# Performance work log

Hardware: AMD Instinct MI355X
Metric: run time of the kernel (lower is better)

Reference implementation:

```python
import jax, jax.numpy as jnp
import numpy as np

N_QUBITS = 12
N_LAYERS = 2
IN_DIM = 16
BATCH = 4096
EPS = 1e-6
C64 = jnp.complex64


def _rz(t):
    return jnp.diag(jnp.stack([jnp.exp(-0.5j * t), jnp.exp(0.5j * t)]).astype(C64))


def _ry(t):
    c = jnp.cos(0.5 * t); s = jnp.sin(0.5 * t)
    return jnp.stack([jnp.stack([c, -s]), jnp.stack([s, c])]).astype(C64)


def _su2(p):
    # SU2: RZ(p0) then RY(p1) then RZ(p2)  ->  U = RZ(p2) @ RY(p1) @ RZ(p0)
    return _rz(p[2]) @ _ry(p[1]) @ _rz(p[0])


def _ising_xx(t):
    c = jnp.cos(0.5 * t).astype(C64); is_ = (-1j * jnp.sin(0.5 * t)).astype(C64)
    M = jnp.zeros((4, 4), C64)
    M = M.at[(0, 1, 2, 3), (0, 1, 2, 3)].set(c)
    M = M.at[(0, 1, 2, 3), (3, 2, 1, 0)].set(is_)
    return M


def _ising_yy(t):
    c = jnp.cos(0.5 * t).astype(C64); is_ = (-1j * jnp.sin(0.5 * t)).astype(C64)
    M = jnp.zeros((4, 4), C64)
    M = M.at[(0, 1, 2, 3), (0, 1, 2, 3)].set(c)
    M = M.at[(1, 2), (2, 1)].set(is_)
    M = M.at[(0, 3), (3, 0)].set(-is_)
    return M


def _ising_zz(t):
    sign = jnp.array([1.0, -1.0, -1.0, 1.0])
    return jnp.diag(jnp.exp(-0.5j * t * sign).astype(C64))


def _apply_1q(state, U, w):
    # state: [B] + [2]*n ; U: [2,2] (shared) or [B,2,2] (per-sample)
    st = jnp.moveaxis(state, w + 1, -1)
    if U.ndim == 2:
        st = jnp.einsum('...i,ji->...j', st, U)
    else:
        st = jnp.einsum('b...i,bji->b...j', st, U)
    return jnp.moveaxis(st, -1, w + 1)


def _apply_2q(state, U, w0, w1):
    st = jnp.moveaxis(state, (w0 + 1, w1 + 1), (-2, -1))
    shp = st.shape
    st = st.reshape(shp[:-2] + (4,))
    st = jnp.einsum('...i,ji->...j', st, U)
    return jnp.moveaxis(st.reshape(shp), (-2, -1), (w0 + 1, w1 + 1))


def _apply_zz_batched(state, theta, w0, w1):
    # IsingZZ is diagonal: multiply by per-sample phases, no matmul needed
    st = jnp.moveaxis(state, (w0 + 1, w1 + 1), (-2, -1))
    sign = jnp.array([[1.0, -1.0], [-1.0, 1.0]])
    ph = jnp.exp(-0.5j * theta[:, None, None] * sign).astype(C64)
    ph = ph.reshape((ph.shape[0],) + (1,) * (st.ndim - 3) + (2, 2))
    return jnp.moveaxis(st * ph, (-2, -1), (w0 + 1, w1 + 1))


def _forward(x, W, b, params):
    n = N_QUBITS
    B = x.shape[0]
    qfeat = x @ W.T + b  # NQE linear front-end -> [B, n_qubits] angles
    state = jnp.zeros((B, 2 ** n), C64).at[:, 0].set(1.0).reshape((B,) + (2,) * n)
    # --- data embedding (n_layers repetitions of RY + nearest-neighbor IsingZZ) ---
    c = jnp.cos(0.5 * qfeat); s = jnp.sin(0.5 * qfeat)
    for _ in range(N_LAYERS):
        for q in range(n):
            U = jnp.stack([jnp.stack([c[:, q], -s[:, q]], -1),
                           jnp.stack([s[:, q], c[:, q]], -1)], -2).astype(C64)  # [B,2,2]
            state = _apply_1q(state, U, q)
        for q in range(n - 1):
            state = _apply_zz_batched(state, qfeat[:, q] * qfeat[:, q + 1], q, q + 1)
    # --- SU4 brickwork ansatz (shared params across batch) ---
    g1 = n // 2; g2 = (n - 1) // 2
    layout = [(2 * i, 2 * i + 1) for i in range(g1)] + [(2 * i + 1, 2 * i + 2) for i in range(g2)]
    p = 0
    for a, bq in layout:
        pp = params[p:p + 15]; p += 15
        state = _apply_1q(state, _su2(pp[0:3]), a)
        state = _apply_1q(state, _su2(pp[3:6]), bq)
        state = _apply_2q(state, _ising_xx(pp[6]), a, bq)   # cartan_sign='ising'
        state = _apply_2q(state, _ising_yy(pp[7]), a, bq)
        state = _apply_2q(state, _ising_zz(pp[8]), a, bq)
        state = _apply_1q(state, _su2(pp[9:12]), a)
        state = _apply_1q(state, _su2(pp[12:15]), bq)
    state = _apply_1q(state, _su2(params[p:p + 3]), 0)
    # <Z_0> = P(q0=0) - P(q0=1)
    probs = jnp.sum(jnp.abs(state.reshape(B, 2, -1)) ** 2, axis=-1)
    y = (probs[:, 0] - probs[:, 1] + 1.0) * 0.5
    return jnp.clip(y, EPS, 1.0 - EPS)


def setup_inputs():
    key = jax.random.key(0)
    k1, k2, k3 = jax.random.split(key, 3)
    x = jax.random.normal(k1, (BATCH, IN_DIM), jnp.float32)
    W = jax.random.normal(k2, (N_QUBITS, IN_DIM), jnp.float32) * 0.3
    b = jnp.zeros((N_QUBITS,), jnp.float32)
    n_params = 15 * (N_QUBITS // 2 + (N_QUBITS - 1) // 2) + 3  # = 168
    params = jax.random.normal(k3, (n_params,), jnp.float32) * 0.1
    return {"x": x, "W": W, "b": b, "params": params}


def reference(x, W, b, params):
    return _forward(x, W, b, params)
```

## Files before the change

kernel.cpp:

```cpp
#include <hip/hip_runtime.h>
#include <math.h>

#define TPB 256

__device__ __forceinline__ float2 cmul(float2 a, float2 b) {
    return make_float2(a.x*b.x - a.y*b.y, a.x*b.y + a.y*b.x);
}
__device__ __forceinline__ float2 cadd(float2 a, float2 b) {
    return make_float2(a.x + b.x, a.y + b.y);
}
__device__ __forceinline__ float2 cfma2(float2 a, float2 b, float2 c) {
    c.x = fmaf(a.x, b.x, fmaf(-a.y, b.y, c.x));
    c.y = fmaf(a.x, b.y, fmaf( a.y, b.x, c.y));
    return c;
}

__device__ __forceinline__ void build_su2(const float* __restrict__ p, float2 U[2][2]) {
    float sb, cb;
    sincosf(0.5f * p[1], &sb, &cb);
    float ap = 0.5f * (p[0] + p[2]);
    float am = 0.5f * (p[0] - p[2]);
    float sap, cap, sam, cam;
    sincosf(ap, &sap, &cap);
    sincosf(am, &sam, &cam);
    U[0][0] = make_float2( cb * cap, -cb * sap);
    U[0][1] = make_float2(-sb * cam, -sb * sam);
    U[1][0] = make_float2( sb * cam, -sb * sam);
    U[1][1] = make_float2( cb * cap,  cb * sap);
}

__global__ __launch_bounds__(TPB) void qcnn_fused(
    const float* __restrict__ x,
    const float* __restrict__ W,
    const float* __restrict__ bias,
    const float* __restrict__ params,
    float* __restrict__ out,
    int n)
{
    __shared__ float2 sE[16];
    __shared__ float  sM[4];

    const int t   = threadIdx.x;
    const int tid = blockIdx.x * TPB + t;
    const int row = (tid < n) ? tid : (n - 1);

    const float* xr = x + row * 16;
    const float4 xv0 = *(const float4*)(xr + 0);
    const float4 xv1 = *(const float4*)(xr + 4);
    const float4 xv2 = *(const float4*)(xr + 8);
    const float4 xv3 = *(const float4*)(xr + 12);
    float qf[4];
    #pragma unroll
    for (int q = 0; q < 4; ++q) {
        const float* wr = W + q * 16;
        float acc = bias[q];
        acc = fmaf(xv0.x, wr[0],  acc); acc = fmaf(xv0.y, wr[1],  acc);
        acc = fmaf(xv0.z, wr[2],  acc); acc = fmaf(xv0.w, wr[3],  acc);
        acc = fmaf(xv1.x, wr[4],  acc); acc = fmaf(xv1.y, wr[5],  acc);
        acc = fmaf(xv1.z, wr[6],  acc); acc = fmaf(xv1.w, wr[7],  acc);
        acc = fmaf(xv2.x, wr[8],  acc); acc = fmaf(xv2.y, wr[9],  acc);
        acc = fmaf(xv2.z, wr[10], acc); acc = fmaf(xv2.w, wr[11], acc);
        acc = fmaf(xv3.x, wr[12], acc); acc = fmaf(xv3.y, wr[13], acc);
        acc = fmaf(xv3.z, wr[14], acc); acc = fmaf(xv3.w, wr[15], acc);
        qf[q] = acc;
    }
    float c[4], s[4];
    #pragma unroll
    for (int q = 0; q < 4; ++q) sincosf(0.5f * qf[q], &s[q], &c[q]);
    float zs01, zc01, zs12, zc12, zs23, zc23;
    sincosf(0.5f * qf[0] * qf[1], &zs01, &zc01);
    sincosf(0.5f * qf[1] * qf[2], &zs12, &zc12);
    sincosf(0.5f * qf[2] * qf[3], &zs23, &zc23);
    const float2 f01e = make_float2(zc01, -zs01), f01d = make_float2(zc01, zs01);
    const float2 f12e = make_float2(zc12, -zs12), f12d = make_float2(zc12, zs12);
    const float2 f23e = make_float2(zc23, -zs23), f23d = make_float2(zc23, zs23);

    if (t < 16) {
        const float* pp = params;
        float2 A1[2][2], B1[2][2], A2[2][2], B2[2][2];
        build_su2(pp + 0,  A1);
        build_su2(pp + 3,  B1);
        build_su2(pp + 9,  A2);
        build_su2(pp + 12, B2);
        const float thx = pp[6], thy = pp[7], thz = pp[8];
        float Sa, Ca, Sb, Cb, sz, cz;
        sincosf(0.5f * (thx - thy), &Sa, &Ca);
        sincosf(0.5f * (thx + thy), &Sb, &Cb);
        sincosf(0.5f * thz, &sz, &cz);
        const float2 pz  = make_float2(cz, -sz);
        const float2 pzc = make_float2(cz,  sz);
        const float2 K00 = make_float2(Ca * pz.x,  Ca * pz.y);
        const float2 K03 = cmul(make_float2(0.f, -Sa), pz);
        const float2 K11 = make_float2(Cb * pzc.x, Cb * pzc.y);
        const float2 K12 = cmul(make_float2(0.f, -Sb), pzc);

        const int r = t >> 2, cc = t & 3;
        float2 T0c[4];
        #pragma unroll
        for (int j = 0; j < 4; ++j)
            T0c[j] = cmul(A1[j >> 1][cc >> 1], B1[j & 1][cc & 1]);
        float2 M1c[4];
        M1c[0] = cadd(cmul(K00, T0c[0]), cmul(K03, T0c[3]));
        M1c[1] = cadd(cmul(K11, T0c[1]), cmul(K12, T0c[2]));
        M1c[2] = cadd(cmul(K12, T0c[1]), cmul(K11, T0c[2]));
        M1c[3] = cadd(cmul(K03, T0c[0]), cmul(K00, T0c[3]));
        float2 acc = make_float2(0.f, 0.f);
        #pragma unroll
        for (int k = 0; k < 4; ++k)
            acc = cfma2(cmul(A2[r >> 1][k >> 1], B2[r & 1][k & 1]), M1c[k], acc);
        sE[t] = acc;
    } else if (t == 16) {
        float2 F[2][2];
        build_su2(params + 165, F);
        const float n00 = F[0][0].x*F[0][0].x + F[0][0].y*F[0][0].y;
        const float n10 = F[1][0].x*F[1][0].x + F[1][0].y*F[1][0].y;
        const float n01 = F[0][1].x*F[0][1].x + F[0][1].y*F[0][1].y;
        const float n11 = F[1][1].x*F[1][1].x + F[1][1].y*F[1][1].y;
        sM[0] = n00 - n10;
        sM[1] = n01 - n11;
        sM[2] = (F[0][0].x*F[0][1].x + F[0][0].y*F[0][1].y)
              - (F[1][0].x*F[1][1].x + F[1][0].y*F[1][1].y);
        sM[3] = (F[0][0].x*F[0][1].y - F[0][0].y*F[0][1].x)
              - (F[1][0].x*F[1][1].y - F[1][0].y*F[1][1].x);
    }
    __syncthreads();

    float2 E[16];
    #pragma unroll
    for (int e = 0; e < 16; ++e) E[e] = sE[e];
    const float m00 = sM[0], m11 = sM[1], mr = sM[2], mi = sM[3];

    float ar[16], ai[16];
    #pragma unroll
    for (int i = 0; i < 16; ++i) {
        const int b0 = (i >> 3) & 1, b1 = (i >> 2) & 1, b2 = (i >> 1) & 1, b3 = i & 1;
        float mag = (b0 ? s[0] : c[0]) * (b1 ? s[1] : c[1])
                  * (b2 ? s[2] : c[2]) * (b3 ? s[3] : c[3]);
        float2 ph = cmul(cmul(b0 == b1 ? f01e : f01d,
                              b1 == b2 ? f12e : f12d),
                         b2 == b3 ? f23e : f23d);
        ar[i] = mag * ph.x;
        ai[i] = mag * ph.y;
    }

    #pragma unroll
    for (int p = 0; p < 16; ++p) if (!(p & 8)) {
        const int q = p | 8;
        float lr = ar[p], li = ai[p], hr = ar[q], hi = ai[q];
        ar[p] = fmaf(c[0], lr, -s[0] * hr);  ai[p] = fmaf(c[0], li, -s[0] * hi);
        ar[q] = fmaf(s[0], lr,  c[0] * hr);  ai[q] = fmaf(s[0], li,  c[0] * hi);
    }
    #pragma unroll
    for (int p = 0; p < 16; ++p) if (!(p & 4)) {
        const int q = p | 4;
        float lr = ar[p], li = ai[p], hr = ar[q], hi = ai[q];
        ar[p] = fmaf(c[1], lr, -s[1] * hr);  ai[p] = fmaf(c[1], li, -s[1] * hi);
        ar[q] = fmaf(s[1], lr,  c[1] * hr);  ai[q] = fmaf(s[1], li,  c[1] * hi);
    }
    #pragma unroll
    for (int p = 0; p < 16; ++p) if (!(p & 2)) {
        const int q = p | 2;
        float lr = ar[p], li = ai[p], hr = ar[q], hi = ai[q];
        ar[p] = fmaf(c[2], lr, -s[2] * hr);  ai[p] = fmaf(c[2], li, -s[2] * hi);
        ar[q] = fmaf(s[2], lr,  c[2] * hr);  ai[q] = fmaf(s[2], li,  c[2] * hi);
    }

    #pragma unroll
    for (int i = 0; i < 16; ++i) {
        const int b0 = (i >> 3) & 1, b1 = (i >> 2) & 1, b2 = (i >> 1) & 1;
        float2 gp = cmul(b0 == b1 ? f01e : f01d, b1 == b2 ? f12e : f12d);
        float nr = ar[i] * gp.x - ai[i] * gp.y;
        float ni = ar[i] * gp.y + ai[i] * gp.x;
        ar[i] = nr; ai[i] = ni;
    }

    #pragma unroll
    for (int gq = 0; gq < 4; ++gq) {
        float xrv[4], xiv[4];
        #pragma unroll
        for (int v = 0; v < 4; ++v) { xrv[v] = ar[(v << 2) | gq]; xiv[v] = ai[(v << 2) | gq]; }
        #pragma unroll
        for (int r = 0; r < 4; ++r) {
            float yr = 0.f, yi = 0.f;
            #pragma unroll
            for (int v = 0; v < 4; ++v) {
                const float2 m = E[r * 4 + v];
                yr = fmaf(m.x, xrv[v], fmaf(-m.y, xiv[v], yr));
                yi = fmaf(m.x, xiv[v], fmaf( m.y, xrv[v], yi));
            }
            ar[(r << 2) | gq] = yr;
            ai[(r << 2) | gq] = yi;
        }
    }

    float d = 0.f;
    #pragma unroll
    for (int i = 0; i < 8; ++i) {
        const float lr = ar[i], li = ai[i], hr = ar[i + 8], hi = ai[i + 8];
        float cross = mr * (lr * hr + li * hi) - mi * (lr * hi - li * hr);
        d += m00 * (lr * lr + li * li) + m11 * (hr * hr + hi * hi) + 2.f * cross;
    }
    float y = 0.5f * (d + 1.0f);
    y = fminf(fmaxf(y, 1e-6f), 1.0f - 1e-6f);
    if (tid < n) out[tid] = y;
}

extern "C" void kernel_launch(void* const* d_in, const int* in_sizes, int n_in,
                              void* d_out, int out_size, void* d_ws, size_t ws_size,
                              hipStream_t stream) {
    (void)in_sizes; (void)n_in; (void)d_ws; (void)ws_size;
    const float* x      = (const float*)d_in[0];
    const float* W      = (const float*)d_in[1];
    const float* bias   = (const float*)d_in[2];
    const float* params = (const float*)d_in[3];
    float* out = (float*)d_out;
    hipLaunchKernelGGL(qcnn_fused, dim3((out_size + TPB - 1) / TPB), dim3(TPB), 0, stream,
                       x, W, bias, params, out, out_size);
}
```

Measured before the change: 14.66 us.

## Use fast intrinsic trig, precompute shared phase products, shrink block size

Every sincosf call is replaced with the __sinf/__cosf hardware intrinsics, which avoids the full-precision range-reduction path. The per-amplitude phase and magnitude products are precomputed once into small tables instead of being rebuilt for each of the 16 amplitudes. The block size drops from 256 to 64, giving 64 blocks over the batch for better CU spread. Fast trig loses accuracy for large arguments, and the ZZ angle products of the input features could be large enough to matter.

```diff
diff --git a/kernel.cpp b/kernel.cpp
--- a/kernel.cpp
+++ b/kernel.cpp
@@ -1,7 +1,7 @@
 #include <hip/hip_runtime.h>
 #include <math.h>
 
-#define TPB 256
+#define TPB 64
 
 __device__ __forceinline__ float2 cmul(float2 a, float2 b) {
     return make_float2(a.x*b.x - a.y*b.y, a.x*b.y + a.y*b.x);
@@ -16,13 +16,11 @@
 }
 
 __device__ __forceinline__ void build_su2(const float* __restrict__ p, float2 U[2][2]) {
-    float sb, cb;
-    sincosf(0.5f * p[1], &sb, &cb);
+    float sb = __sinf(0.5f * p[1]), cb = __cosf(0.5f * p[1]);
     float ap = 0.5f * (p[0] + p[2]);
     float am = 0.5f * (p[0] - p[2]);
-    float sap, cap, sam, cam;
-    sincosf(ap, &sap, &cap);
-    sincosf(am, &sam, &cam);
+    float sap = __sinf(ap), cap = __cosf(ap);
+    float sam = __sinf(am), cam = __cosf(am);
     U[0][0] = make_float2( cb * cap, -cb * sap);
     U[0][1] = make_float2(-sb * cam, -sb * sam);
     U[1][0] = make_float2( sb * cam, -sb * sam);
@@ -66,11 +64,16 @@
     }
     float c[4], s[4];
     #pragma unroll
-    for (int q = 0; q < 4; ++q) sincosf(0.5f * qf[q], &s[q], &c[q]);
-    float zs01, zc01, zs12, zc12, zs23, zc23;
-    sincosf(0.5f * qf[0] * qf[1], &zs01, &zc01);
-    sincosf(0.5f * qf[1] * qf[2], &zs12, &zc12);
-    sincosf(0.5f * qf[2] * qf[3], &zs23, &zc23);
+    for (int q = 0; q < 4; ++q) {
+        s[q] = __sinf(0.5f * qf[q]);
+        c[q] = __cosf(0.5f * qf[q]);
+    }
+    const float h01 = 0.5f * qf[0] * qf[1];
+    const float h12 = 0.5f * qf[1] * qf[2];
+    const float h23 = 0.5f * qf[2] * qf[3];
+    const float zs01 = __sinf(h01), zc01 = __cosf(h01);
+    const float zs12 = __sinf(h12), zc12 = __cosf(h12);
+    const float zs23 = __sinf(h23), zc23 = __cosf(h23);
     const float2 f01e = make_float2(zc01, -zs01), f01d = make_float2(zc01, zs01);
     const float2 f12e = make_float2(zc12, -zs12), f12d = make_float2(zc12, zs12);
     const float2 f23e = make_float2(zc23, -zs23), f23d = make_float2(zc23, zs23);
@@ -83,10 +86,10 @@
         build_su2(pp + 9,  A2);
         build_su2(pp + 12, B2);
         const float thx = pp[6], thy = pp[7], thz = pp[8];
-        float Sa, Ca, Sb, Cb, sz, cz;
-        sincosf(0.5f * (thx - thy), &Sa, &Ca);
-        sincosf(0.5f * (thx + thy), &Sb, &Cb);
-        sincosf(0.5f * thz, &sz, &cz);
+        const float ha = 0.5f * (thx - thy), hb = 0.5f * (thx + thy), hz = 0.5f * thz;
+        const float Sa = __sinf(ha), Ca = __cosf(ha);
+        const float Sb = __sinf(hb), Cb = __cosf(hb);
+        const float sz = __sinf(hz), cz = __cosf(hz);
         const float2 pz  = make_float2(cz, -sz);
         const float2 pzc = make_float2(cz,  sz);
         const float2 K00 = make_float2(Ca * pz.x,  Ca * pz.y);
@@ -130,15 +133,27 @@
     for (int e = 0; e < 16; ++e) E[e] = sE[e];
     const float m00 = sM[0], m11 = sM[1], mr = sM[2], mi = sM[3];
 
+    float2 p0112[4];
+    p0112[0] = cmul(f01d, f12d);
+    p0112[1] = cmul(f01d, f12e);
+    p0112[2] = cmul(f01e, f12d);
+    p0112[3] = cmul(f01e, f12e);
+    float2 p8[8];
+    #pragma unroll
+    for (int k = 0; k < 4; ++k) {
+        p8[2*k]     = cmul(p0112[k], f23d);
+        p8[2*k + 1] = cmul(p0112[k], f23e);
+    }
+    const float m01v[4] = { c[0]*c[1], c[0]*s[1], s[0]*c[1], s[0]*s[1] };
+    const float m23v[4] = { c[2]*c[3], c[2]*s[3], s[2]*c[3], s[2]*s[3] };
+
     float ar[16], ai[16];
     #pragma unroll
     for (int i = 0; i < 16; ++i) {
         const int b0 = (i >> 3) & 1, b1 = (i >> 2) & 1, b2 = (i >> 1) & 1, b3 = i & 1;
-        float mag = (b0 ? s[0] : c[0]) * (b1 ? s[1] : c[1])
-                  * (b2 ? s[2] : c[2]) * (b3 ? s[3] : c[3]);
-        float2 ph = cmul(cmul(b0 == b1 ? f01e : f01d,
-                              b1 == b2 ? f12e : f12d),
-                         b2 == b3 ? f23e : f23d);
+        const int eq01 = (b0 == b1), eq12 = (b1 == b2), eq23 = (b2 == b3);
+        const float mag = m01v[i >> 2] * m23v[i & 3];
+        const float2 ph = p8[(eq01 << 2) | (eq12 << 1) | eq23];
         ar[i] = mag * ph.x;
         ai[i] = mag * ph.y;
     }
@@ -168,9 +183,9 @@
     #pragma unroll
     for (int i = 0; i < 16; ++i) {
         const int b0 = (i >> 3) & 1, b1 = (i >> 2) & 1, b2 = (i >> 1) & 1;
-        float2 gp = cmul(b0 == b1 ? f01e : f01d, b1 == b2 ? f12e : f12d);
-        float nr = ar[i] * gp.x - ai[i] * gp.y;
-        float ni = ar[i] * gp.y + ai[i] * gp.x;
+        const float2 gp = p0112[((b0 == b1) << 1) | (b1 == b2)];
+        const float nr = ar[i] * gp.x - ai[i] * gp.y;
+        const float ni = ar[i] * gp.y + ai[i] * gp.x;
         ar[i] = nr; ai[i] = ni;
     }
 
@@ -197,7 +212,7 @@
     #pragma unroll
     for (int i = 0; i < 8; ++i) {
         const float lr = ar[i], li = ai[i], hr = ar[i + 8], hi = ai[i + 8];
-        float cross = mr * (lr * hr + li * hi) - mi * (lr * hi - li * hr);
+        const float cross = mr * (lr * hr + li * hi) - mi * (lr * hi - li * hr);
         d += m00 * (lr * lr + li * li) + m11 * (hr * hr + hi * hi) + 2.f * cross;
     }
     float y = 0.5f * (d + 1.0f);
```

Measured after the change: 17.47 us. 1.19x slower.
